# Kernel tuning notes

Measured on AMD Instinct MI355X. Metric: run time of the kernel, lower is better.

Reference implementation:

```python
import jax, jax.numpy as jnp
import numpy as np

NUM_VECTORS = 8192
DIM = 64

def setup_inputs() -> dict:
    key = jax.random.key(0)
    kx, kw = jax.random.split(key)
    x = jax.random.normal(kx, (8, 4096, DIM), dtype=jnp.float32)
    W = jax.random.normal(kw, (NUM_VECTORS, DIM), dtype=jnp.float32)
    return {"x": x, "W": W}

def reference(x, W):
    # x: [B, S, C] channels_last (ndim==3 -> channels_first=False)
    shape = x.shape
    flat = x.reshape(-1, shape[-1])  # [N, C]
    # cdist + argmin: argmin of squared euclidean distance is identical to argmin of cdist
    x2 = jnp.sum(flat * flat, axis=1, keepdims=True)          # [N, 1]
    w2 = jnp.sum(W * W, axis=1)                                # [K]
    d2 = x2 - 2.0 * (flat @ W.T) + w2                          # [N, K] dominant intermediate
    indices = jnp.argmin(d2, axis=1)                           # [N]
    z = W[indices]                                             # gather [N, C]
    # losses (use_ema=True -> codebook_loss = 0)
    commitment_loss = jnp.mean((z - jax.lax.stop_gradient(flat)) ** 2)
    codebook_loss = jnp.zeros_like(commitment_loss)
    # straight-through estimator
    z_st = flat + jax.lax.stop_gradient(z - flat)
    # perplexity: scatter one-hot counts -> mean -> entropy
    n = flat.shape[0]
    counts = jnp.zeros((NUM_VECTORS,), dtype=jnp.float32).at[indices].add(1.0)
    avg_probs = counts / n
    perplexity = jnp.exp(-jnp.sum(avg_probs * jnp.log(avg_probs + 1e-10)))
    z_out = z_st.reshape(shape)
    return (z_out, codebook_loss, commitment_loss, perplexity)
```

## Files before the change

### kernel.cpp

```cpp
#include <hip/hip_runtime.h>
#include <math.h>

#define N_ROWS 32768
#define K_CODES 8192
#define DIM 64
#define CHUNKS 4
#define CPC (K_CODES / CHUNKS)
#define TILES (CPC / 32)

using half8  = __attribute__((ext_vector_type(8))) _Float16;
using f32x16 = __attribute__((ext_vector_type(16))) float;

#define WS_W2     0
#define WS_COUNTS 32768
#define WS_CSUM   65536
#define WS_BEST   65552
#define WS_X2     327696
#define WS_WHL    458768

__device__ __forceinline__ void gload_lds16(const _Float16* g, _Float16* l) {
    __builtin_amdgcn_global_load_lds(
        (const __attribute__((address_space(1))) void*)g,
        (__attribute__((address_space(3))) void*)l, 16, 0, 0);
}

__global__ __launch_bounds__(256) void vq_prep(const float* __restrict__ W,
                                               const float* __restrict__ x,
                                               _Float16* __restrict__ whl,
                                               float* __restrict__ w2g,
                                               float* __restrict__ x2g,
                                               unsigned long long* __restrict__ best,
                                               int* __restrict__ counts,
                                               float* __restrict__ csum) {
    int g = blockIdx.x * 256 + threadIdx.x;
    int code = g >> 6, k = g & 63;
    float w = W[g];
    _Float16 h  = (_Float16)w;
    _Float16 lo = (_Float16)(w - (float)h);
    whl[(size_t)code * 128 + k]      = h;
    whl[(size_t)code * 128 + 64 + k] = lo;
    float s = w * w;
    #pragma unroll
    for (int off = 32; off; off >>= 1) s += __shfl_down(s, off);
    if (k == 0) w2g[code] = s;
    float4 xv = *(const float4*)(x + (size_t)g * 4);
    float ss = xv.x * xv.x + xv.y * xv.y + xv.z * xv.z + xv.w * xv.w;
    #pragma unroll
    for (int off = 8; off; off >>= 1) ss += __shfl_down(ss, off);
    if ((g & 15) == 0) x2g[g >> 4] = ss;
    if (g < N_ROWS)  best[g] = ~0ULL;
    if (g < K_CODES) counts[g] = 0;
    if (g == 0)      *csum = 0.f;
}

__global__ __launch_bounds__(256, 4) void vq_mfma(const float* __restrict__ x,
                                                  const _Float16* __restrict__ whl,
                                                  const float* __restrict__ w2g,
                                                  unsigned long long* __restrict__ best) {
    __shared__ __align__(16) _Float16 lds[2][4096];
    __shared__ float w2l[CPC];

    const int t     = threadIdx.x;
    const int wv    = t >> 6;
    const int l     = t & 63;
    const int ln31  = l & 31;
    const int lhalf = l >> 5;
    const int chunk = blockIdx.x & (CHUNKS - 1);
    const int rblk  = blockIdx.x / CHUNKS;
    const int rowb  = rblk * 128 + wv * 32;
    const int cbase = chunk * CPC;

    for (int i = t; i < CPC; i += 256) w2l[i] = w2g[cbase + i];

    half8 ahi[4], alo[4];
    {
        const float* xr = x + (size_t)(rowb + ln31) * DIM + lhalf * 8;
        #pragma unroll
        for (int kt = 0; kt < 4; ++kt) {
            float4 a0 = *(const float4*)(xr + kt * 16);
            float4 a1 = *(const float4*)(xr + kt * 16 + 4);
            float fa[8] = {a0.x, a0.y, a0.z, a0.w, a1.x, a1.y, a1.z, a1.w};
            #pragma unroll
            for (int j = 0; j < 8; ++j) {
                _Float16 h = (_Float16)fa[j];
                ahi[kt][j] = h;
                alo[kt][j] = (_Float16)(fa[j] - (float)h);
            }
        }
    }

    const _Float16* srcp[2];
    int ldsG[2];
    #pragma unroll
    for (int p = 0; p < 2; ++p) {
        int q = p * 4 + wv;
        srcp[p] = whl + (size_t)(cbase + ln31) * 128 + ((q & 1) * 8 + lhalf + 2 * (q >> 1)) * 8;
        ldsG[p] = (p * 256 + wv * 64) * 8;
    }

    float bv[16];
    int   bi[16];
    #pragma unroll
    for (int s2 = 0; s2 < 16; ++s2) { bv[s2] = 3.4e38f; bi[s2] = 0; }

    #pragma unroll
    for (int p = 0; p < 2; ++p) gload_lds16(srcp[p], &lds[0][0] + ldsG[p]);
    __syncthreads();

    int cur = 0;
    for (int tile = 0; tile < TILES; ++tile) {
        if (tile < TILES - 1) {
            #pragma unroll
            for (int p = 0; p < 2; ++p)
                gload_lds16(srcp[p] + (tile + 1) * 4096, &lds[0][0] + (cur ^ 1) * 4096 + ldsG[p]);
        }
        const float w2v = w2l[tile * 32 + ln31];
        const _Float16* lb = &lds[0][0] + cur * 4096;

        f32x16 accA = {}, accB = {};
        __builtin_amdgcn_s_setprio(1);
        #pragma unroll
        for (int kt = 0; kt < 4; ++kt) {
            half8 bh = *(const half8*)(lb + ((kt * 2 + 0) * 64 + l) * 8);
            half8 bl = *(const half8*)(lb + ((kt * 2 + 1) * 64 + l) * 8);
            accA = __builtin_amdgcn_mfma_f32_32x32x16_f16(ahi[kt], bh, accA, 0, 0, 0);
            accB = __builtin_amdgcn_mfma_f32_32x32x16_f16(alo[kt], bh, accB, 0, 0, 0);
            accB = __builtin_amdgcn_mfma_f32_32x32x16_f16(ahi[kt], bl, accB, 0, 0, 0);
        }
        __builtin_amdgcn_s_setprio(0);

        const int cc = cbase + tile * 32 + ln31;
        #pragma unroll
        for (int s2 = 0; s2 < 16; ++s2) {
            float sA = fmaf(-2.f, accA[s2], fmaf(-2.f, accB[s2], w2v));
            if (sA < bv[s2]) { bv[s2] = sA; bi[s2] = cc; }
        }
        __syncthreads();
        cur ^= 1;
    }

    #pragma unroll
    for (int s2 = 0; s2 < 16; ++s2) {
        unsigned uk = __float_as_uint(bv[s2]);
        uk = (uk >> 31) ? ~uk : (uk | 0x80000000u);
        unsigned long long key = ((unsigned long long)uk << 32) | (unsigned)bi[s2];
        #pragma unroll
        for (int off = 16; off; off >>= 1) {
            unsigned long long o = __shfl_xor(key, off);
            key = (o < key) ? o : key;
        }
        if (ln31 == 0) {
            int rl = (s2 & 3) + 8 * (s2 >> 2) + 4 * lhalf;
            atomicMin(&best[rowb + rl], key);
        }
    }
}

__global__ __launch_bounds__(256) void vq_gather(const float* __restrict__ W,
                                                 const unsigned long long* __restrict__ best,
                                                 const float* __restrict__ x2g,
                                                 float* __restrict__ zout,
                                                 int* __restrict__ counts,
                                                 float* __restrict__ csum) {
    int t   = threadIdx.x;
    int row = blockIdx.x * 64 + (t >> 2);
    int seg = t & 3;
    unsigned long long key = best[row];
    int idx = (int)(key & 0xFFFFFFFFULL);

    const float* wrow = W    + (size_t)idx * DIM + seg * 16;
    float*       zrow = zout + (size_t)row * DIM + seg * 16;
    #pragma unroll
    for (int j = 0; j < 16; j += 4) *(float4*)(zrow + j) = *(const float4*)(wrow + j);

    float local = 0.f;
    if (seg == 0) {
        atomicAdd(&counts[idx], 1);
        unsigned uk = (unsigned)(key >> 32);
        unsigned ob = (uk & 0x80000000u) ? (uk & 0x7FFFFFFFu) : ~uk;
        local = x2g[row] + __uint_as_float(ob);
    }
    #pragma unroll
    for (int off = 32; off; off >>= 1) local += __shfl_down(local, off);
    if ((t & 63) == 0) atomicAdd(csum, local);
}

__global__ __launch_bounds__(256) void vq_final(const int* __restrict__ counts,
                                                const float* __restrict__ csum,
                                                float* __restrict__ out3) {
    __shared__ float sh[4];
    float e = 0.f;
    for (int i = threadIdx.x; i < K_CODES; i += 256) {
        float p = (float)counts[i] * (1.0f / N_ROWS);
        e += p * logf(p + 1e-10f);
    }
    #pragma unroll
    for (int off = 32; off; off >>= 1) e += __shfl_down(e, off);
    if ((threadIdx.x & 63) == 0) sh[threadIdx.x >> 6] = e;
    __syncthreads();
    if (threadIdx.x == 0) {
        float tot = sh[0] + sh[1] + sh[2] + sh[3];
        out3[0] = 0.f;
        out3[1] = csum[0] * (1.0f / ((float)N_ROWS * DIM));
        out3[2] = expf(-tot);
    }
}

extern "C" void kernel_launch(void* const* d_in, const int* in_sizes, int n_in,
                              void* d_out, int out_size, void* d_ws, size_t ws_size,
                              hipStream_t stream) {
    (void)in_sizes; (void)n_in; (void)out_size; (void)ws_size;
    const float* x = (const float*)d_in[0];
    const float* W = (const float*)d_in[1];
    float* zout = (float*)d_out;
    float* out3 = (float*)d_out + (size_t)N_ROWS * DIM;

    float*              w2g    = (float*)((char*)d_ws + WS_W2);
    int*                counts = (int*)((char*)d_ws + WS_COUNTS);
    float*              csum   = (float*)((char*)d_ws + WS_CSUM);
    unsigned long long* best   = (unsigned long long*)((char*)d_ws + WS_BEST);
    float*              x2g    = (float*)((char*)d_ws + WS_X2);
    _Float16*           whl    = (_Float16*)((char*)d_ws + WS_WHL);

    vq_prep  <<<K_CODES * DIM / 256,     256, 0, stream>>>(W, x, whl, w2g, x2g, best, counts, csum);
    vq_mfma  <<<(N_ROWS / 128) * CHUNKS, 256, 0, stream>>>(x, whl, w2g, best);
    vq_gather<<<N_ROWS / 64,             256, 0, stream>>>(W, best, x2g, zout, counts, csum);
    vq_final <<<1,                       256, 0, stream>>>(counts, csum, out3);
}
```

Before: 160.7 us.

## Fold -2 scale and codebook norms into MFMA, process two tiles per iteration

```diff
diff --git a/kernel.cpp b/kernel.cpp
--- a/kernel.cpp
+++ b/kernel.cpp
@@ -4,19 +4,20 @@
 #define N_ROWS 32768
 #define K_CODES 8192
 #define DIM 64
-#define CHUNKS 4
+#define CHUNKS 8
 #define CPC (K_CODES / CHUNKS)
 #define TILES (CPC / 32)
+#define ITERS (TILES / 2)
 
 using half8  = __attribute__((ext_vector_type(8))) _Float16;
 using f32x16 = __attribute__((ext_vector_type(16))) float;
 
-#define WS_W2     0
+#define WS_W2HL   0
 #define WS_COUNTS 32768
 #define WS_CSUM   65536
 #define WS_BEST   65552
 #define WS_X2     327696
-#define WS_WHL    458768
+#define WS_WM2    458768
 
 __device__ __forceinline__ void gload_lds16(const _Float16* g, _Float16* l) {
     __builtin_amdgcn_global_load_lds(
@@ -26,8 +27,8 @@
 
 __global__ __launch_bounds__(256) void vq_prep(const float* __restrict__ W,
                                                const float* __restrict__ x,
-                                               _Float16* __restrict__ whl,
-                                               float* __restrict__ w2g,
+                                               _Float16* __restrict__ wm2hl,
+                                               unsigned* __restrict__ w2hl,
                                                float* __restrict__ x2g,
                                                unsigned long long* __restrict__ best,
                                                int* __restrict__ counts,
@@ -35,14 +36,21 @@
     int g = blockIdx.x * 256 + threadIdx.x;
     int code = g >> 6, k = g & 63;
     float w = W[g];
-    _Float16 h  = (_Float16)w;
-    _Float16 lo = (_Float16)(w - (float)h);
-    whl[(size_t)code * 128 + k]      = h;
-    whl[(size_t)code * 128 + 64 + k] = lo;
+    float wm2 = -2.0f * w;
+    _Float16 h  = (_Float16)wm2;
+    _Float16 lo = (_Float16)(wm2 - (float)h);
+    wm2hl[(size_t)code * 128 + k]      = h;
+    wm2hl[(size_t)code * 128 + 64 + k] = lo;
     float s = w * w;
     #pragma unroll
     for (int off = 32; off; off >>= 1) s += __shfl_down(s, off);
-    if (k == 0) w2g[code] = s;
+    if (k == 0) {
+        _Float16 wh = (_Float16)s;
+        _Float16 wl = (_Float16)(s - (float)wh);
+        unsigned pk = (unsigned)(unsigned short)__builtin_bit_cast(unsigned short, wh)
+                    | ((unsigned)(unsigned short)__builtin_bit_cast(unsigned short, wl) << 16);
+        w2hl[code] = pk;
+    }
     float4 xv = *(const float4*)(x + (size_t)g * 4);
     float ss = xv.x * xv.x + xv.y * xv.y + xv.z * xv.z + xv.w * xv.w;
     #pragma unroll
@@ -54,11 +62,11 @@
 }
 
 __global__ __launch_bounds__(256, 4) void vq_mfma(const float* __restrict__ x,
-                                                  const _Float16* __restrict__ whl,
-                                                  const float* __restrict__ w2g,
+                                                  const _Float16* __restrict__ wm2hl,
+                                                  const unsigned* __restrict__ w2g,
                                                   unsigned long long* __restrict__ best) {
-    __shared__ __align__(16) _Float16 lds[2][4096];
-    __shared__ float w2l[CPC];
+    __shared__ __align__(16) _Float16 lds[4][4096];
+    __shared__ unsigned w2lds[CPC];
 
     const int t     = threadIdx.x;
     const int wv    = t >> 6;
@@ -70,7 +78,7 @@
     const int rowb  = rblk * 128 + wv * 32;
     const int cbase = chunk * CPC;
 
-    for (int i = t; i < CPC; i += 256) w2l[i] = w2g[cbase + i];
+    for (int i = t; i < CPC; i += 256) w2lds[i] = w2g[cbase + i];
 
     half8 ahi[4], alo[4];
     {
@@ -89,12 +97,16 @@
         }
     }
 
+    half8 aw2;
+    #pragma unroll
+    for (int j = 0; j < 8; ++j) aw2[j] = (lhalf == 0 && j < 2) ? (_Float16)1.0f : (_Float16)0.0f;
+
     const _Float16* srcp[2];
     int ldsG[2];
     #pragma unroll
     for (int p = 0; p < 2; ++p) {
         int q = p * 4 + wv;
-        srcp[p] = whl + (size_t)(cbase + ln31) * 128 + ((q & 1) * 8 + lhalf + 2 * (q >> 1)) * 8;
+        srcp[p] = wm2hl + (size_t)(cbase + ln31) * 128 + ((q & 1) * 8 + lhalf + 2 * (q >> 1)) * 8;
         ldsG[p] = (p * 256 + wv * 64) * 8;
     }
 
@@ -103,41 +115,60 @@
     #pragma unroll
     for (int s2 = 0; s2 < 16; ++s2) { bv[s2] = 3.4e38f; bi[s2] = 0; }
 
-    #pragma unroll
-    for (int p = 0; p < 2; ++p) gload_lds16(srcp[p], &lds[0][0] + ldsG[p]);
+#define STAGE(tt)                                                                \
+    { _Pragma("unroll")                                                          \
+      for (int p = 0; p < 2; ++p)                                                \
+          gload_lds16(srcp[p] + (size_t)(tt) * 4096,                             \
+                      &lds[(tt) & 3][0] + ldsG[p]); }
+
+    STAGE(0)
+    STAGE(1)
     __syncthreads();
 
-    int cur = 0;
-    for (int tile = 0; tile < TILES; ++tile) {
-        if (tile < TILES - 1) {
-            #pragma unroll
-            for (int p = 0; p < 2; ++p)
-                gload_lds16(srcp[p] + (tile + 1) * 4096, &lds[0][0] + (cur ^ 1) * 4096 + ldsG[p]);
-        }
-        const float w2v = w2l[tile * 32 + ln31];
-        const _Float16* lb = &lds[0][0] + cur * 4096;
-
-        f32x16 accA = {}, accB = {};
+    for (int it = 0; it < ITERS; ++it) {
+        const int tA = 2 * it, tB = 2 * it + 1;
+        if (it < ITERS - 1) { STAGE(tA + 2) STAGE(tB + 2) }
+
+        const _Float16* lbA = &lds[tA & 3][0];
+        const _Float16* lbB = &lds[tB & 3][0];
+
+        unsigned pkA = w2lds[tA * 32 + ln31];
+        unsigned pkB = w2lds[tB * 32 + ln31];
+        union { half8 h8; unsigned u[4]; } bwA, bwB;
+        bwA.u[0] = (lhalf == 0) ? pkA : 0u; bwA.u[1] = 0; bwA.u[2] = 0; bwA.u[3] = 0;
+        bwB.u[0] = (lhalf == 0) ? pkB : 0u; bwB.u[1] = 0; bwB.u[2] = 0; bwB.u[3] = 0;
+
+        f32x16 acc0 = {}, acc1 = {};
         __builtin_amdgcn_s_setprio(1);
+        acc0 = __builtin_amdgcn_mfma_f32_32x32x16_f16(aw2, bwA.h8, acc0, 0, 0, 0);
+        acc1 = __builtin_amdgcn_mfma_f32_32x32x16_f16(aw2, bwB.h8, acc1, 0, 0, 0);
         #pragma unroll
         for (int kt = 0; kt < 4; ++kt) {
-            half8 bh = *(const half8*)(lb + ((kt * 2 + 0) * 64 + l) * 8);
-            half8 bl = *(const half8*)(lb + ((kt * 2 + 1) * 64 + l) * 8);
-            accA = __builtin_amdgcn_mfma_f32_32x32x16_f16(ahi[kt], bh, accA, 0, 0, 0);
-            accB = __builtin_amdgcn_mfma_f32_32x32x16_f16(alo[kt], bh, accB, 0, 0, 0);
-            accB = __builtin_amdgcn_mfma_f32_32x32x16_f16(ahi[kt], bl, accB, 0, 0, 0);
+            half8 bhA = *(const half8*)(lbA + ((kt * 2 + 0) * 64 + l) * 8);
+            half8 blA = *(const half8*)(lbA + ((kt * 2 + 1) * 64 + l) * 8);
+            half8 bhB = *(const half8*)(lbB + ((kt * 2 + 0) * 64 + l) * 8);
+            half8 blB = *(const half8*)(lbB + ((kt * 2 + 1) * 64 + l) * 8);
+            acc0 = __builtin_amdgcn_mfma_f32_32x32x16_f16(ahi[kt], bhA, acc0, 0, 0, 0);
+            acc1 = __builtin_amdgcn_mfma_f32_32x32x16_f16(ahi[kt], bhB, acc1, 0, 0, 0);
+            acc0 = __builtin_amdgcn_mfma_f32_32x32x16_f16(alo[kt], bhA, acc0, 0, 0, 0);
+            acc1 = __builtin_amdgcn_mfma_f32_32x32x16_f16(alo[kt], bhB, acc1, 0, 0, 0);
+            acc0 = __builtin_amdgcn_mfma_f32_32x32x16_f16(ahi[kt], blA, acc0, 0, 0, 0);
+            acc1 = __builtin_amdgcn_mfma_f32_32x32x16_f16(ahi[kt], blB, acc1, 0, 0, 0);
         }
         __builtin_amdgcn_s_setprio(0);
 
-        const int cc = cbase + tile * 32 + ln31;
+        const int ccA = cbase + tA * 32 + ln31;
+        const int ccB = cbase + tB * 32 + ln31;
         #pragma unroll
         for (int s2 = 0; s2 < 16; ++s2) {
-            float sA = fmaf(-2.f, accA[s2], fmaf(-2.f, accB[s2], w2v));
-            if (sA < bv[s2]) { bv[s2] = sA; bi[s2] = cc; }
+            float sA = acc0[s2];
+            float sB = acc1[s2];
+            if (sA < bv[s2]) { bv[s2] = sA; bi[s2] = ccA; }
+            if (sB < bv[s2]) { bv[s2] = sB; bi[s2] = ccB; }
         }
         __syncthreads();
-        cur ^= 1;
-    }
+    }
+#undef STAGE
 
     #pragma unroll
     for (int s2 = 0; s2 < 16; ++s2) {
@@ -215,15 +246,15 @@
     float* zout = (float*)d_out;
     float* out3 = (float*)d_out + (size_t)N_ROWS * DIM;
 
-    float*              w2g    = (float*)((char*)d_ws + WS_W2);
+    unsigned*           w2hl   = (unsigned*)((char*)d_ws + WS_W2HL);
     int*                counts = (int*)((char*)d_ws + WS_COUNTS);
     float*              csum   = (float*)((char*)d_ws + WS_CSUM);
     unsigned long long* best   = (unsigned long long*)((char*)d_ws + WS_BEST);
     float*              x2g    = (float*)((char*)d_ws + WS_X2);
-    _Float16*           whl    = (_Float16*)((char*)d_ws + WS_WHL);
-
-    vq_prep  <<<K_CODES * DIM / 256,     256, 0, stream>>>(W, x, whl, w2g, x2g, best, counts, csum);
-    vq_mfma  <<<(N_ROWS / 128) * CHUNKS, 256, 0, stream>>>(x, whl, w2g, best);
+    _Float16*           wm2hl  = (_Float16*)((char*)d_ws + WS_WM2);
+
+    vq_prep  <<<K_CODES * DIM / 256,     256, 0, stream>>>(W, x, wm2hl, w2hl, x2g, best, counts, csum);
+    vq_mfma  <<<(N_ROWS / 128) * CHUNKS, 256, 0, stream>>>(x, wm2hl, w2hl, best);
     vq_gather<<<N_ROWS / 64,             256, 0, stream>>>(W, best, x2g, zout, counts, csum);
     vq_final <<<1,                       256, 0, stream>>>(counts, csum, out3);
 }
```

After: 160.7 us. Within noise of the previous version (+0.0%).

## Deepen codebook LDS pipeline to 4-stage ring and parallelize final reduction

Applied to the files above, without the earlier changes.

```diff
diff --git a/kernel.cpp b/kernel.cpp
--- a/kernel.cpp
+++ b/kernel.cpp
@@ -14,6 +14,8 @@
 #define WS_W2     0
 #define WS_COUNTS 32768
 #define WS_CSUM   65536
+#define WS_ESUM   65540
+#define WS_DONE   65544
 #define WS_BEST   65552
 #define WS_X2     327696
 #define WS_WHL    458768
@@ -31,7 +33,8 @@
                                                float* __restrict__ x2g,
                                                unsigned long long* __restrict__ best,
                                                int* __restrict__ counts,
-                                               float* __restrict__ csum) {
+                                               float* __restrict__ scal,
+                                               int* __restrict__ done) {
     int g = blockIdx.x * 256 + threadIdx.x;
     int code = g >> 6, k = g & 63;
     float w = W[g];
@@ -50,14 +53,14 @@
     if ((g & 15) == 0) x2g[g >> 4] = ss;
     if (g < N_ROWS)  best[g] = ~0ULL;
     if (g < K_CODES) counts[g] = 0;
-    if (g == 0)      *csum = 0.f;
+    if (g == 0) { scal[0] = 0.f; scal[1] = 0.f; *done = 0; }
 }
 
 __global__ __launch_bounds__(256, 4) void vq_mfma(const float* __restrict__ x,
                                                   const _Float16* __restrict__ whl,
                                                   const float* __restrict__ w2g,
                                                   unsigned long long* __restrict__ best) {
-    __shared__ __align__(16) _Float16 lds[2][4096];
+    __shared__ __align__(16) _Float16 ring[4][4096];
     __shared__ float w2l[CPC];
 
     const int t     = threadIdx.x;
@@ -103,41 +106,48 @@
     #pragma unroll
     for (int s2 = 0; s2 < 16; ++s2) { bv[s2] = 3.4e38f; bi[s2] = 0; }
 
-    #pragma unroll
-    for (int p = 0; p < 2; ++p) gload_lds16(srcp[p], &lds[0][0] + ldsG[p]);
+#define STAGE(tt)                                                                \
+    { _Pragma("unroll")                                                          \
+      for (int p = 0; p < 2; ++p)                                                \
+          gload_lds16(srcp[p] + (size_t)(tt) * 4096,                             \
+                      &ring[(tt) & 3][0] + ldsG[p]); }
+
+    STAGE(0) STAGE(1) STAGE(2)
     __syncthreads();
 
-    int cur = 0;
-    for (int tile = 0; tile < TILES; ++tile) {
-        if (tile < TILES - 1) {
-            #pragma unroll
-            for (int p = 0; p < 2; ++p)
-                gload_lds16(srcp[p] + (tile + 1) * 4096, &lds[0][0] + (cur ^ 1) * 4096 + ldsG[p]);
-        }
-        const float w2v = w2l[tile * 32 + ln31];
-        const _Float16* lb = &lds[0][0] + cur * 4096;
-
-        f32x16 accA = {}, accB = {};
-        __builtin_amdgcn_s_setprio(1);
-        #pragma unroll
-        for (int kt = 0; kt < 4; ++kt) {
-            half8 bh = *(const half8*)(lb + ((kt * 2 + 0) * 64 + l) * 8);
-            half8 bl = *(const half8*)(lb + ((kt * 2 + 1) * 64 + l) * 8);
-            accA = __builtin_amdgcn_mfma_f32_32x32x16_f16(ahi[kt], bh, accA, 0, 0, 0);
-            accB = __builtin_amdgcn_mfma_f32_32x32x16_f16(alo[kt], bh, accB, 0, 0, 0);
-            accB = __builtin_amdgcn_mfma_f32_32x32x16_f16(ahi[kt], bl, accB, 0, 0, 0);
-        }
-        __builtin_amdgcn_s_setprio(0);
-
-        const int cc = cbase + tile * 32 + ln31;
-        #pragma unroll
-        for (int s2 = 0; s2 < 16; ++s2) {
-            float sA = fmaf(-2.f, accA[s2], fmaf(-2.f, accB[s2], w2v));
-            if (sA < bv[s2]) { bv[s2] = sA; bi[s2] = cc; }
-        }
-        __syncthreads();
-        cur ^= 1;
-    }
+#define TILE_BODY(VM, DO_STAGE, tt)                                              \
+  {                                                                              \
+    asm volatile("s_waitcnt vmcnt(" #VM ")" ::: "memory");                       \
+    __builtin_amdgcn_s_barrier();                                                \
+    if (DO_STAGE) { STAGE((tt) + 3) }  \
+    const _Float16* lb = &ring[(tt) & 3][0];                                     \
+    const float w2v = w2l[(tt) * 32 + ln31];                                     \
+    f32x16 acc = {};                                                             \
+    __builtin_amdgcn_s_setprio(1);                                               \
+    _Pragma("unroll")                                                            \
+    for (int kt = 0; kt < 4; ++kt) {                                             \
+      half8 bh = *(const half8*)(lb + ((kt * 2 + 0) * 64 + l) * 8);              \
+      half8 bl = *(const half8*)(lb + ((kt * 2 + 1) * 64 + l) * 8);              \
+      acc = __builtin_amdgcn_mfma_f32_32x32x16_f16(ahi[kt], bh, acc, 0, 0, 0);   \
+      acc = __builtin_amdgcn_mfma_f32_32x32x16_f16(alo[kt], bh, acc, 0, 0, 0);   \
+      acc = __builtin_amdgcn_mfma_f32_32x32x16_f16(ahi[kt], bl, acc, 0, 0, 0);   \
+    }                                                                            \
+    __builtin_amdgcn_s_setprio(0);                                               \
+    const int cc = cbase + (tt) * 32 + ln31;                                     \
+    _Pragma("unroll")                                                            \
+    for (int s2 = 0; s2 < 16; ++s2) {                                            \
+      float sA = fmaf(-2.f, acc[s2], w2v);                                       \
+      if (sA < bv[s2]) { bv[s2] = sA; bi[s2] = cc; }                             \
+    }                                                                            \
+  }
+
+    for (int tile = 0; tile < TILES - 3; ++tile)
+        TILE_BODY(4, true, tile);
+    TILE_BODY(4, false, TILES - 3);
+    TILE_BODY(2, false, TILES - 2);
+    TILE_BODY(0, false, TILES - 1);
+#undef TILE_BODY
+#undef STAGE
 
     #pragma unroll
     for (int s2 = 0; s2 < 16; ++s2) {
@@ -186,23 +196,28 @@
 }
 
 __global__ __launch_bounds__(256) void vq_final(const int* __restrict__ counts,
-                                                const float* __restrict__ csum,
+                                                float* __restrict__ scal,
+                                                int* __restrict__ done,
                                                 float* __restrict__ out3) {
     __shared__ float sh[4];
-    float e = 0.f;
-    for (int i = threadIdx.x; i < K_CODES; i += 256) {
-        float p = (float)counts[i] * (1.0f / N_ROWS);
-        e += p * logf(p + 1e-10f);
-    }
+    int g = blockIdx.x * 256 + threadIdx.x;
+    float p = (float)counts[g] * (1.0f / N_ROWS);
+    float e = p * logf(p + 1e-10f);
     #pragma unroll
     for (int off = 32; off; off >>= 1) e += __shfl_down(e, off);
     if ((threadIdx.x & 63) == 0) sh[threadIdx.x >> 6] = e;
     __syncthreads();
     if (threadIdx.x == 0) {
-        float tot = sh[0] + sh[1] + sh[2] + sh[3];
-        out3[0] = 0.f;
-        out3[1] = csum[0] * (1.0f / ((float)N_ROWS * DIM));
-        out3[2] = expf(-tot);
+        atomicAdd(&scal[1], sh[0] + sh[1] + sh[2] + sh[3]);
+        __threadfence();
+        int old = atomicAdd(done, 1);
+        if (old == 31) {
+            float es = atomicAdd(&scal[1], 0.f);
+            float cs = atomicAdd(&scal[0], 0.f);
+            out3[0] = 0.f;
+            out3[1] = cs * (1.0f / ((float)N_ROWS * DIM));
+            out3[2] = expf(-es);
+        }
     }
 }
 
@@ -217,13 +232,14 @@
 
     float*              w2g    = (float*)((char*)d_ws + WS_W2);
     int*                counts = (int*)((char*)d_ws + WS_COUNTS);
-    float*              csum   = (float*)((char*)d_ws + WS_CSUM);
+    float*              scal   = (float*)((char*)d_ws + WS_CSUM);
+    int*                done   = (int*)((char*)d_ws + WS_DONE);
     unsigned long long* best   = (unsigned long long*)((char*)d_ws + WS_BEST);
     float*              x2g    = (float*)((char*)d_ws + WS_X2);
     _Float16*           whl    = (_Float16*)((char*)d_ws + WS_WHL);
 
-    vq_prep  <<<K_CODES * DIM / 256,     256, 0, stream>>>(W, x, whl, w2g, x2g, best, counts, csum);
+    vq_prep  <<<K_CODES * DIM / 256,     256, 0, stream>>>(W, x, whl, w2g, x2g, best, counts, scal, done);
     vq_mfma  <<<(N_ROWS / 128) * CHUNKS, 256, 0, stream>>>(x, whl, w2g, best);
-    vq_gather<<<N_ROWS / 64,             256, 0, stream>>>(W, best, x2g, zout, counts, csum);
-    vq_final <<<1,                       256, 0, stream>>>(counts, csum, out3);
-}
+    vq_gather<<<N_ROWS / 64,             256, 0, stream>>>(W, best, x2g, zout, counts, &scal[0]);
+    vq_final <<<K_CODES / 256,           256, 0, stream>>>(counts, scal, done, out3);
+}
```

After: 152.0 us. 1.06x faster.
